# Kernel tuning notes

Measured on AMD Instinct MI355X. Metric: run time of the kernel, lower is better.

The kernel has to match this reference:

```python
import jax, jax.numpy as jnp
import numpy as np

NUM_ENTITIES = 100000
NUM_RELATIONS = 1000
BATCH = 65536
NUM_NEGS = 64
NUM_TRUE = 1000000


def _hash_triples(t):
    # matches torch: h = e0 << 42 | r << 21 | e2 (ids < 2^21 so no overlap)
    t = t.astype(jnp.int64)
    return (t[:, 0] << 42) | (t[:, 1] << 21) | t[:, 2]


def setup_inputs() -> dict:
    key = jax.random.key(0)
    k1, k2, k3, k4, k5 = jax.random.split(key, 5)
    # positive triples: entities in [1, NUM_ENTITIES), relations in [0, NUM_RELATIONS)
    heads = jax.random.randint(k1, (BATCH,), 1, NUM_ENTITIES, dtype=jnp.int64)
    rels = jax.random.randint(k2, (BATCH,), 0, NUM_RELATIONS, dtype=jnp.int64)
    tails = jax.random.randint(k3, (BATCH,), 1, NUM_ENTITIES, dtype=jnp.int64)
    positive_batch = jnp.stack([heads, rels, tails], axis=1)
    total = BATCH * NUM_NEGS
    # pre-drawn uniform candidates in [1, NUM_ENTITIES) (pad_idx=0 excluded by construction)
    rand_vals = jax.random.randint(k4, (total,), 1, NUM_ENTITIES, dtype=jnp.int64)
    # filter table: sorted unique hashes of training triples (built on host, like buffer init)
    rng = np.random.default_rng(0)
    true = np.stack([
        rng.integers(1, NUM_ENTITIES, NUM_TRUE),
        rng.integers(0, NUM_RELATIONS, NUM_TRUE),
        rng.integers(1, NUM_ENTITIES, NUM_TRUE),
    ], axis=1).astype(np.int64)
    h = (true[:, 0] << 42) | (true[:, 1] << 21) | true[:, 2]
    hashes_sorted = jnp.asarray(np.sort(np.unique(h)))
    return {
        "positive_batch": positive_batch,
        "rand_vals": rand_vals,
        "hashes_sorted": hashes_sorted,
        "num_negs_per_pos": NUM_NEGS,
    }


def reference(positive_batch, rand_vals, hashes_sorted, num_negs_per_pos):
    B = positive_batch.shape[0]
    total = B * num_negs_per_pos
    # repeat_interleave(num_negs, dim=0)
    neg = jnp.repeat(positive_batch, num_negs_per_pos, axis=0)  # [total, 3]
    # corruption scheme [head, tail]: first ceil(total/2) rows corrupt col 0, rest col 2
    split = -(-total // 2)
    col_idx = jnp.where(jnp.arange(total) < split, 0, 2)  # [total]
    orig = jnp.take_along_axis(neg, col_idx[:, None], axis=1)[:, 0]  # [total]
    # pad_idx == 0 fast path: rng in [1, max_index); shift past the original value
    shift = ((rand_vals >= orig) & (orig > 0)).astype(rand_vals.dtype)
    repl = rand_vals + shift
    neg = neg.at[jnp.arange(total), col_idx].set(repl)
    # SortedHashTripleFilter: True = keep (triple not in training set)
    h = _hash_triples(neg)
    L = hashes_sorted.shape[0]
    pos = jnp.searchsorted(hashes_sorted, h)
    in_set = (pos < L) & (hashes_sorted[jnp.clip(pos, 0, L - 1)] == h)
    keep = ~in_set
    return neg.reshape(B, num_negs_per_pos, 3), keep.reshape(B, num_negs_per_pos)
```

## Files before the change

kernel.cpp:

```cpp
#include <hip/hip_runtime.h>

typedef long long i64;
typedef unsigned long long u64;


template <typename T>
__device__ __forceinline__ bool interp_member(const T* __restrict__ table,
                                              int L, u64 key) {
    u64 v0 = (u64)table[0];
    u64 vN = (u64)table[L - 1];
    if (key <= v0) return key == v0;
    if (key >= vN) return key == vN;
    int lo = 0, hi = L - 1;
    u64 vlo = v0, vhi = vN;
    for (int it = 0; it < 12 && hi - lo > 8; ++it) {
        float f = (float)(key - vlo) * __builtin_amdgcn_rcpf((float)(vhi - vlo));
        int mid = lo + (int)(f * (float)(hi - lo));
        if (mid <= lo) mid = lo + 1;
        if (mid >= hi) mid = hi - 1;
        u64 v = (u64)table[mid];
        if (v == key) return true;
        if (v < key) { lo = mid; vlo = v; }
        else         { hi = mid; vhi = v; }
    }
    while (hi - lo > 8) {
        int mid = lo + ((hi - lo) >> 1);
        u64 v = (u64)table[mid];
        if (v == key) return true;
        if (v < key) lo = mid; else hi = mid;
    }
    bool eq = false;
    for (int j = lo + 1; j < hi; ++j) eq |= ((u64)table[j] == key);
    return eq;
}

template <typename T>
__device__ __forceinline__ void sample_body(
    const T* __restrict__ pos, const T* __restrict__ rand_vals,
    const T* __restrict__ table,
    int* __restrict__ out_neg, int* __restrict__ out_keep,
    unsigned i, int split, int L, unsigned num_negs)
{
    unsigned b = i / num_negs;
    i64 h = (i64)pos[3 * b + 0];
    i64 r = (i64)pos[3 * b + 1];
    i64 t = (i64)pos[3 * b + 2];
    i64 rv = (i64)rand_vals[i];

    const bool corrupt_head = (i < (unsigned)split);
    i64 orig = corrupt_head ? h : t;
    i64 repl = rv + (((rv >= orig) & (orig > 0)) ? 1 : 0);
    if (corrupt_head) h = repl; else t = repl;

    u64 key = ((u64)h << 42) | ((u64)r << 21) | (u64)t;
    bool in_set = interp_member(table, L, key);

    out_neg[3 * (size_t)i + 0] = (int)h;
    out_neg[3 * (size_t)i + 1] = (int)r;
    out_neg[3 * (size_t)i + 2] = (int)t;
    out_keep[i] = in_set ? 0 : 1;
}

__global__ __launch_bounds__(256) void neg_sample_kernel(
    const void* __restrict__ pos, const void* __restrict__ rand_vals,
    const void* __restrict__ table,
    int* __restrict__ out_neg, int* __restrict__ out_keep,
    int total, int split, int L, unsigned num_negs)
{
    unsigned i = blockIdx.x * blockDim.x + threadIdx.x;
    if (i >= (unsigned)total) return;

    const int* pw = (const int*)pos;
    const bool is64 = (pw[3] == 0);

    if (is64) {
        sample_body<i64>((const i64*)pos, (const i64*)rand_vals, (const i64*)table,
                         out_neg, out_keep, i, split, L, num_negs);
    } else {
        sample_body<int>((const int*)pos, (const int*)rand_vals, (const int*)table,
                         out_neg, out_keep, i, split, L, num_negs);
    }
}

extern "C" void kernel_launch(void* const* d_in, const int* in_sizes, int n_in,
                              void* d_out, int out_size, void* d_ws, size_t ws_size,
                              hipStream_t stream) {
    const void* pos       = d_in[0];
    const void* rand_vals = d_in[1];
    const void* table     = d_in[2];

    const int B     = in_sizes[0] / 3;
    const int total = in_sizes[1];
    const int L     = in_sizes[2];
    const unsigned num_negs = (unsigned)(total / B);
    const int split = (total + 1) / 2;

    int* out_neg  = (int*)d_out;
    int* out_keep = out_neg + (size_t)total * 3;

    const int threads = 256;
    const int blocks  = (total + threads - 1) / threads;
    neg_sample_kernel<<<blocks, threads, 0, stream>>>(
        pos, rand_vals, table, out_neg, out_keep, total, split, L, num_negs);
}
```

Before: 96.85 us.

## Process four samples per thread with interleaved interpolation searches

Each thread now handles four consecutive negatives. It runs their interpolation-search steps in lockstep so several dependent table loads are in flight at once, which is meant to hide memory latency. Output triples are written as three int4 stores, and the final scan becomes a fixed 7-element unrolled probe. In exchange the thread count drops fourfold and register pressure rises, which may cut occupancy. The int4 stores hard-code K_ITEMS=4 and assume 16-byte alignment of out_neg.

Measured after the change: 157.0 us. 62.1% more time.

```diff
diff --git a/kernel.cpp b/kernel.cpp
--- a/kernel.cpp
+++ b/kernel.cpp
@@ -2,6 +2,11 @@
 
 typedef long long i64;
 typedef unsigned long long u64;
+
+
+#ifndef K_ITEMS
+#define K_ITEMS 4
+#endif
 
 
 template <typename T>
@@ -61,24 +66,156 @@
     out_keep[i] = in_set ? 0 : 1;
 }
 
+
+template <typename T>
+__device__ __forceinline__ void sample_body_k(
+    const T* __restrict__ pos, const T* __restrict__ rand_vals,
+    const T* __restrict__ table,
+    int* __restrict__ out_neg, int* __restrict__ out_keep,
+    unsigned i0, int split, int L, unsigned num_negs)
+{
+    u64 v0 = (u64)table[0];
+    u64 vN = (u64)table[L - 1];
+
+    unsigned b;
+    if ((num_negs & (num_negs - 1)) == 0u) b = i0 >> __builtin_ctz(num_negs);
+    else                                   b = i0 / num_negs;
+    unsigned r_in_b = i0 - b * num_negs;
+
+    i64 ph = (i64)pos[3 * (size_t)b + 0];
+    i64 pr = (i64)pos[3 * (size_t)b + 1];
+    i64 pt = (i64)pos[3 * (size_t)b + 2];
+
+    u64 key[K_ITEMS];
+    int lo[K_ITEMS], hi[K_ITEMS];
+    u64 vlo[K_ITEMS], vhi[K_ITEMS];
+    bool found[K_ITEMS], act[K_ITEMS];
+    int hv[K_ITEMS], rv2[K_ITEMS], tv[K_ITEMS];
+
+    #pragma unroll
+    for (int k = 0; k < K_ITEMS; ++k) {
+        if (k > 0) {
+            ++r_in_b;
+            if (r_in_b == num_negs) {
+                r_in_b = 0; ++b;
+                ph = (i64)pos[3 * (size_t)b + 0];
+                pr = (i64)pos[3 * (size_t)b + 1];
+                pt = (i64)pos[3 * (size_t)b + 2];
+            }
+        }
+        unsigned i = i0 + (unsigned)k;
+        i64 h = ph, r = pr, t = pt;
+        i64 rv = (i64)rand_vals[i];
+
+        const bool corrupt_head = (i < (unsigned)split);
+        i64 orig = corrupt_head ? h : t;
+        i64 repl = rv + (((rv >= orig) & (orig > 0)) ? 1 : 0);
+        if (corrupt_head) h = repl; else t = repl;
+
+        u64 kk = ((u64)h << 42) | ((u64)r << 21) | (u64)t;
+        key[k] = kk;
+        hv[k] = (int)h; rv2[k] = (int)r; tv[k] = (int)t;
+
+        found[k] = (kk == v0) | (kk == vN);
+        act[k]   = (kk > v0) & (kk < vN);
+        lo[k] = 0; hi[k] = L - 1; vlo[k] = v0; vhi[k] = vN;
+    }
+
+    {
+        int4* np4 = (int4*)(out_neg + 3 * (size_t)i0);
+        np4[0] = make_int4(hv[0], rv2[0], tv[0], hv[1]);
+        np4[1] = make_int4(rv2[1], tv[1], hv[2], rv2[2]);
+        np4[2] = make_int4(tv[2], hv[3], rv2[3], tv[3]);
+    }
+
+    #pragma unroll 1
+    for (int it = 0; it < 12; ++it) {
+        if (!(act[0] | act[1] | act[2] | act[3])) break;
+        int mid[K_ITEMS];
+        u64 v[K_ITEMS];
+        #pragma unroll
+        for (int k = 0; k < K_ITEMS; ++k) {
+            float num = (float)(key[k] - vlo[k]);
+            float den = (float)(vhi[k] - vlo[k]);
+            float f = num * __builtin_amdgcn_rcpf(den);
+            f = fminf(fmaxf(f, 0.0f), 1.0f);
+            int m = lo[k] + (int)(f * (float)(hi[k] - lo[k]));
+            if (m <= lo[k]) m = lo[k] + 1;
+            if (m >= hi[k]) m = hi[k] - 1;
+            mid[k] = m;
+            v[k] = (u64)table[m];
+        }
+        #pragma unroll
+        for (int k = 0; k < K_ITEMS; ++k) {
+            if (act[k]) {
+                if (v[k] == key[k])     { found[k] = true; act[k] = false; }
+                else if (v[k] < key[k]) { lo[k] = mid[k]; vlo[k] = v[k]; }
+                else                    { hi[k] = mid[k]; vhi[k] = v[k]; }
+                if (hi[k] - lo[k] <= 8) act[k] = false;
+            }
+        }
+    }
+
+    #pragma unroll
+    for (int k = 0; k < K_ITEMS; ++k) {
+        while (hi[k] - lo[k] > 8) {
+            int m = lo[k] + ((hi[k] - lo[k]) >> 1);
+            u64 v = (u64)table[m];
+            if (v == key[k]) { found[k] = true; break; }
+            if (v < key[k]) lo[k] = m; else hi[k] = m;
+        }
+    }
+
+    #pragma unroll
+    for (int k = 0; k < K_ITEMS; ++k) {
+        u64 e[7];
+        #pragma unroll
+        for (int j = 0; j < 7; ++j) {
+            int idx = lo[k] + 1 + j;
+            if (idx > L - 1) idx = L - 1;
+            e[j] = (u64)table[idx];
+        }
+        bool eq = false;
+        #pragma unroll
+        for (int j = 0; j < 7; ++j) eq |= (e[j] == key[k]);
+        found[k] |= eq;
+    }
+
+    #pragma unroll
+    for (int k = 0; k < K_ITEMS; ++k)
+        out_keep[i0 + (unsigned)k] = found[k] ? 0 : 1;
+}
+
+
 __global__ __launch_bounds__(256) void neg_sample_kernel(
     const void* __restrict__ pos, const void* __restrict__ rand_vals,
     const void* __restrict__ table,
     int* __restrict__ out_neg, int* __restrict__ out_keep,
     int total, int split, int L, unsigned num_negs)
 {
-    unsigned i = blockIdx.x * blockDim.x + threadIdx.x;
-    if (i >= (unsigned)total) return;
+    unsigned t = blockIdx.x * blockDim.x + threadIdx.x;
+    unsigned i0 = t * (unsigned)K_ITEMS;
+    if (i0 >= (unsigned)total) return;
 
     const int* pw = (const int*)pos;
     const bool is64 = (pw[3] == 0);
 
-    if (is64) {
-        sample_body<i64>((const i64*)pos, (const i64*)rand_vals, (const i64*)table,
-                         out_neg, out_keep, i, split, L, num_negs);
+    if (i0 + (unsigned)K_ITEMS <= (unsigned)total) {
+        if (is64) sample_body_k<i64>((const i64*)pos, (const i64*)rand_vals,
+                                     (const i64*)table, out_neg, out_keep,
+                                     i0, split, L, num_negs);
+        else      sample_body_k<int>((const int*)pos, (const int*)rand_vals,
+                                     (const int*)table, out_neg, out_keep,
+                                     i0, split, L, num_negs);
     } else {
-        sample_body<int>((const int*)pos, (const int*)rand_vals, (const int*)table,
-                         out_neg, out_keep, i, split, L, num_negs);
+        for (unsigned i = i0; i < (unsigned)total; ++i) {
+            if (is64) sample_body<i64>((const i64*)pos, (const i64*)rand_vals,
+                                       (const i64*)table, out_neg, out_keep,
+                                       i, split, L, num_negs);
+            else      sample_body<int>((const int*)pos, (const int*)rand_vals,
+                                       (const int*)table, out_neg, out_keep,
+                                       i, split, L, num_negs);
+        }
     }
 }
 
@@ -99,7 +236,8 @@
     int* out_keep = out_neg + (size_t)total * 3;
 
     const int threads = 256;
-    const int blocks  = (total + threads - 1) / threads;
+    const int items_per_block = threads * K_ITEMS;
+    const int blocks = (total + items_per_block - 1) / items_per_block;
     neg_sample_kernel<<<blocks, threads, 0, stream>>>(
         pos, rand_vals, table, out_neg, out_keep, total, split, L, num_negs);
 }
```
